# Optimization experiments

Hardware: AMD Instinct MI355X
Metric: run time of the kernel (lower is better)

Reference implementation:

```python
import jax, jax.numpy as jnp
import numpy as np

B = 2_000_000
EPS = 1e-8


def setup_inputs() -> dict:
    key = jax.random.key(0)
    k = jax.random.split(key, 6)
    loc1 = jax.random.normal(k[0], (B, 3), dtype=jnp.float32)
    loc2 = jax.random.normal(k[1], (B, 3), dtype=jnp.float32)
    # positive scales so R diag(s) R^T is PSD and the sum is invertible
    scale1 = jax.random.uniform(k[2], (B, 3), dtype=jnp.float32) + 0.1
    scale2 = jax.random.uniform(k[3], (B, 3), dtype=jnp.float32) + 0.1
    rot_matrix1 = jax.random.normal(k[4], (B, 3, 3), dtype=jnp.float32)
    rot_matrix2 = jax.random.normal(k[5], (B, 3, 3), dtype=jnp.float32)
    # cov1/cov2 are placeholders: source recomputes them when non-None
    cov1 = jnp.zeros((B, 3, 3), dtype=jnp.float32)
    cov2 = jnp.zeros((B, 3, 3), dtype=jnp.float32)
    return dict(loc1=loc1, scale1=scale1, rot_matrix1=rot_matrix1,
                loc2=loc2, scale2=scale2, rot_matrix2=rot_matrix2,
                cov1=cov1, cov2=cov2)


def _cov_from(rot, scale):
    # R @ diag(s) @ R^T, fused: einsum over the diagonal
    return jnp.einsum('bij,bj,bkj->bik', rot, scale, rot)


def reference(loc1, scale1, rot_matrix1, loc2, scale2, rot_matrix2, cov1, cov2):
    # Faithful to source: cov1/cov2 passed non-None => recomputed from rot/scale
    c1 = _cov_from(rot_matrix1, scale1)  # [B,3,3]
    c2 = _cov_from(rot_matrix2, scale2)  # [B,3,3]
    eye = jnp.eye(3, dtype=c1.dtype) * EPS
    K = jnp.matmul(c1, jnp.linalg.inv(c1 + c2 + eye))  # [B,3,3]
    # (loc2-loc1) row-vector times K^T  ==  K @ (loc2-loc1)
    loc_new = loc1 + jnp.einsum('bij,bj->bi', K, loc2 - loc1)  # [B,3]
    cov_new = c1 + jnp.matmul(K, c1)  # [B,3,3]  (sign as in source)
    return (loc_new, cov_new)
```

## Files before the change

### kernel.cpp

```cpp
#include <hip/hip_runtime.h>

#define GM_EPS 1e-8f

__global__ __launch_bounds__(256) void gaussian_merge_kernel(
    const float* __restrict__ loc1,
    const float* __restrict__ scale1,
    const float* __restrict__ rot1,
    const float* __restrict__ loc2,
    const float* __restrict__ scale2,
    const float* __restrict__ rot2,
    float* __restrict__ out_loc,
    float* __restrict__ out_cov,
    int n)
{
    int i = blockIdx.x * blockDim.x + threadIdx.x;
    if (i >= n) return;

    const long ib3 = (long)i * 3;
    const long ib9 = (long)i * 9;

    float l1[3], l2[3], s1[3], s2[3];
#pragma unroll
    for (int k = 0; k < 3; ++k) {
        l1[k] = loc1[ib3 + k];
        l2[k] = loc2[ib3 + k];
        s1[k] = scale1[ib3 + k];
        s2[k] = scale2[ib3 + k];
    }
    float R1[9], R2[9];
#pragma unroll
    for (int k = 0; k < 9; ++k) {
        R1[k] = rot1[ib9 + k];
        R2[k] = rot2[ib9 + k];
    }

    float c1[3][3], S[3][3];
#pragma unroll
    for (int a = 0; a < 3; ++a) {
#pragma unroll
        for (int b = 0; b < 3; ++b) {
            float v1 = 0.f, v2 = 0.f;
#pragma unroll
            for (int k = 0; k < 3; ++k) {
                v1 = fmaf(R1[a * 3 + k] * s1[k], R1[b * 3 + k], v1);
                v2 = fmaf(R2[a * 3 + k] * s2[k], R2[b * 3 + k], v2);
            }
            c1[a][b] = v1;
            S[a][b]  = v1 + v2 + (a == b ? GM_EPS : 0.f);
        }
    }

    const float m00 = S[0][0], m01 = S[0][1], m02 = S[0][2];
    const float m11 = S[1][1], m12 = S[1][2], m22 = S[2][2];
    const float A0 = m11 * m22 - m12 * m12;
    const float A1 = m02 * m12 - m01 * m22;
    const float A2 = m01 * m12 - m02 * m11;
    const float det = m00 * A0 + m01 * A1 + m02 * A2;
    const float invdet = 1.0f / det;

    float Sinv[3][3];
    Sinv[0][0] = A0 * invdet;
    Sinv[0][1] = A1 * invdet;
    Sinv[0][2] = A2 * invdet;
    Sinv[1][1] = (m00 * m22 - m02 * m02) * invdet;
    Sinv[1][2] = (m01 * m02 - m00 * m12) * invdet;
    Sinv[2][2] = (m00 * m11 - m01 * m01) * invdet;
    Sinv[1][0] = Sinv[0][1];
    Sinv[2][0] = Sinv[0][2];
    Sinv[2][1] = Sinv[1][2];

    float K[3][3];
#pragma unroll
    for (int a = 0; a < 3; ++a) {
#pragma unroll
        for (int b = 0; b < 3; ++b) {
            float v = 0.f;
#pragma unroll
            for (int k = 0; k < 3; ++k)
                v = fmaf(c1[a][k], Sinv[k][b], v);
            K[a][b] = v;
        }
    }

    float d0 = l2[0] - l1[0], d1 = l2[1] - l1[1], d2 = l2[2] - l1[2];
#pragma unroll
    for (int a = 0; a < 3; ++a) {
        float v = fmaf(K[a][0], d0, fmaf(K[a][1], d1, K[a][2] * d2));
        out_loc[ib3 + a] = l1[a] + v;
    }

#pragma unroll
    for (int a = 0; a < 3; ++a) {
#pragma unroll
        for (int b = 0; b < 3; ++b) {
            float v = 0.f;
#pragma unroll
            for (int k = 0; k < 3; ++k)
                v = fmaf(K[a][k], c1[k][b], v);
            out_cov[ib9 + a * 3 + b] = c1[a][b] + v;
        }
    }
}

extern "C" void kernel_launch(void* const* d_in, const int* in_sizes, int n_in,
                              void* d_out, int out_size, void* d_ws, size_t ws_size,
                              hipStream_t stream) {
    const float* loc1   = (const float*)d_in[0];
    const float* scale1 = (const float*)d_in[1];
    const float* rot1   = (const float*)d_in[2];
    const float* loc2   = (const float*)d_in[3];
    const float* scale2 = (const float*)d_in[4];
    const float* rot2   = (const float*)d_in[5];

    const int n = in_sizes[0] / 3;

    float* out     = (float*)d_out;
    float* out_loc = out;
    float* out_cov = out + (size_t)n * 3;

    const int block = 256;
    const int grid  = (n + block - 1) / block;
    gaussian_merge_kernel<<<grid, block, 0, stream>>>(
        loc1, scale1, rot1, loc2, scale2, rot2, out_loc, out_cov, n);
}
```

Before: 328.0 us.

## Stage AoS inputs and outputs through LDS with coalesced float4 transfers

Each block now loads its slice of rotations, locations and scales into shared memory with coalesced float4 loads, computes per-thread from LDS, writes results back to LDS, and stores them out with coalesced float4 stores. This replaces the strided per-thread scalar loads and stores over 3- and 9-float records, which waste memory transactions. Block size drops to 128 to bound the LDS footprint. The cost is two barriers and extra LDS traffic, plus possible bank conflicts from the stride-9 and stride-3 LDS accesses.

```diff
diff --git a/kernel.cpp b/kernel.cpp
--- a/kernel.cpp
+++ b/kernel.cpp
@@ -1,8 +1,9 @@
 #include <hip/hip_runtime.h>
 
 #define GM_EPS 1e-8f
+#define BLK 128
 
-__global__ __launch_bounds__(256) void gaussian_merge_kernel(
+__global__ __launch_bounds__(BLK) void gaussian_merge_kernel(
     const float* __restrict__ loc1,
     const float* __restrict__ scale1,
     const float* __restrict__ rot1,
@@ -13,92 +14,141 @@
     float* __restrict__ out_cov,
     int n)
 {
-    int i = blockIdx.x * blockDim.x + threadIdx.x;
-    if (i >= n) return;
+    __shared__ alignas(16) float sR1[BLK * 9];
+    __shared__ alignas(16) float sR2[BLK * 9];
+    __shared__ alignas(16) float sL1[BLK * 3];
+    __shared__ alignas(16) float sL2[BLK * 3];
+    __shared__ alignas(16) float sS1[BLK * 3];
+    __shared__ alignas(16) float sS2[BLK * 3];
 
-    const long ib3 = (long)i * 3;
-    const long ib9 = (long)i * 9;
+    const int  tid       = threadIdx.x;
+    const long blockBase = (long)blockIdx.x * BLK;
+    const int  cnt       = (int)((blockBase + BLK <= (long)n) ? BLK : ((long)n - blockBase));
 
-    float l1[3], l2[3], s1[3], s2[3];
-#pragma unroll
-    for (int k = 0; k < 3; ++k) {
-        l1[k] = loc1[ib3 + k];
-        l2[k] = loc2[ib3 + k];
-        s1[k] = scale1[ib3 + k];
-        s2[k] = scale2[ib3 + k];
-    }
-    float R1[9], R2[9];
-#pragma unroll
-    for (int k = 0; k < 9; ++k) {
-        R1[k] = rot1[ib9 + k];
-        R2[k] = rot2[ib9 + k];
-    }
+    if (cnt == BLK) {
+        const float4* r1 = (const float4*)(rot1 + blockBase * 9);
+        const float4* r2 = (const float4*)(rot2 + blockBase * 9);
+        float4* d1 = (float4*)sR1;
+        float4* d2 = (float4*)sR2;
+        for (int j = tid; j < BLK * 9 / 4; j += BLK) { d1[j] = r1[j]; d2[j] = r2[j]; }
 
-    float c1[3][3], S[3][3];
-#pragma unroll
-    for (int a = 0; a < 3; ++a) {
-#pragma unroll
-        for (int b = 0; b < 3; ++b) {
-            float v1 = 0.f, v2 = 0.f;
-#pragma unroll
-            for (int k = 0; k < 3; ++k) {
-                v1 = fmaf(R1[a * 3 + k] * s1[k], R1[b * 3 + k], v1);
-                v2 = fmaf(R2[a * 3 + k] * s2[k], R2[b * 3 + k], v2);
-            }
-            c1[a][b] = v1;
-            S[a][b]  = v1 + v2 + (a == b ? GM_EPS : 0.f);
+        const float4* p1 = (const float4*)(loc1   + blockBase * 3);
+        const float4* p2 = (const float4*)(loc2   + blockBase * 3);
+        const float4* q1 = (const float4*)(scale1 + blockBase * 3);
+        const float4* q2 = (const float4*)(scale2 + blockBase * 3);
+        float4* e1 = (float4*)sL1;
+        float4* e2 = (float4*)sL2;
+        float4* f1 = (float4*)sS1;
+        float4* f2 = (float4*)sS2;
+        if (tid < BLK * 3 / 4) {
+            e1[tid] = p1[tid]; e2[tid] = p2[tid];
+            f1[tid] = q1[tid]; f2[tid] = q2[tid];
+        }
+    } else {
+        for (int j = tid; j < cnt * 9; j += BLK) {
+            sR1[j] = rot1[blockBase * 9 + j];
+            sR2[j] = rot2[blockBase * 9 + j];
+        }
+        for (int j = tid; j < cnt * 3; j += BLK) {
+            sL1[j] = loc1[blockBase * 3 + j];
+            sL2[j] = loc2[blockBase * 3 + j];
+            sS1[j] = scale1[blockBase * 3 + j];
+            sS2[j] = scale2[blockBase * 3 + j];
         }
     }
+    __syncthreads();
 
-    const float m00 = S[0][0], m01 = S[0][1], m02 = S[0][2];
-    const float m11 = S[1][1], m12 = S[1][2], m22 = S[2][2];
-    const float A0 = m11 * m22 - m12 * m12;
-    const float A1 = m02 * m12 - m01 * m22;
-    const float A2 = m01 * m12 - m02 * m11;
-    const float det = m00 * A0 + m01 * A1 + m02 * A2;
-    const float invdet = 1.0f / det;
+    if (tid < cnt) {
+        float R1[9], R2[9], l1[3], l2[3], s1[3], s2[3];
+#pragma unroll
+        for (int k = 0; k < 9; ++k) { R1[k] = sR1[tid * 9 + k]; R2[k] = sR2[tid * 9 + k]; }
+#pragma unroll
+        for (int k = 0; k < 3; ++k) {
+            l1[k] = sL1[tid * 3 + k];
+            l2[k] = sL2[tid * 3 + k];
+            s1[k] = sS1[tid * 3 + k];
+            s2[k] = sS2[tid * 3 + k];
+        }
 
-    float Sinv[3][3];
-    Sinv[0][0] = A0 * invdet;
-    Sinv[0][1] = A1 * invdet;
-    Sinv[0][2] = A2 * invdet;
-    Sinv[1][1] = (m00 * m22 - m02 * m02) * invdet;
-    Sinv[1][2] = (m01 * m02 - m00 * m12) * invdet;
-    Sinv[2][2] = (m00 * m11 - m01 * m01) * invdet;
-    Sinv[1][0] = Sinv[0][1];
-    Sinv[2][0] = Sinv[0][2];
-    Sinv[2][1] = Sinv[1][2];
+        float c1[3][3], S[3][3];
+#pragma unroll
+        for (int a = 0; a < 3; ++a) {
+#pragma unroll
+            for (int b = 0; b < 3; ++b) {
+                float v1 = 0.f, v2 = 0.f;
+#pragma unroll
+                for (int k = 0; k < 3; ++k) {
+                    v1 = fmaf(R1[a * 3 + k] * s1[k], R1[b * 3 + k], v1);
+                    v2 = fmaf(R2[a * 3 + k] * s2[k], R2[b * 3 + k], v2);
+                }
+                c1[a][b] = v1;
+                S[a][b]  = v1 + v2 + (a == b ? GM_EPS : 0.f);
+            }
+        }
 
-    float K[3][3];
+        const float m00 = S[0][0], m01 = S[0][1], m02 = S[0][2];
+        const float m11 = S[1][1], m12 = S[1][2], m22 = S[2][2];
+        const float A0 = m11 * m22 - m12 * m12;
+        const float A1 = m02 * m12 - m01 * m22;
+        const float A2 = m01 * m12 - m02 * m11;
+        const float det    = m00 * A0 + m01 * A1 + m02 * A2;
+        const float invdet = 1.0f / det;
+
+        float Sinv[3][3];
+        Sinv[0][0] = A0 * invdet;
+        Sinv[0][1] = A1 * invdet;
+        Sinv[0][2] = A2 * invdet;
+        Sinv[1][1] = (m00 * m22 - m02 * m02) * invdet;
+        Sinv[1][2] = (m01 * m02 - m00 * m12) * invdet;
+        Sinv[2][2] = (m00 * m11 - m01 * m01) * invdet;
+        Sinv[1][0] = Sinv[0][1];
+        Sinv[2][0] = Sinv[0][2];
+        Sinv[2][1] = Sinv[1][2];
+
+        float K[3][3];
 #pragma unroll
-    for (int a = 0; a < 3; ++a) {
+        for (int a = 0; a < 3; ++a) {
 #pragma unroll
-        for (int b = 0; b < 3; ++b) {
-            float v = 0.f;
+            for (int b = 0; b < 3; ++b) {
+                float v = 0.f;
 #pragma unroll
-            for (int k = 0; k < 3; ++k)
-                v = fmaf(c1[a][k], Sinv[k][b], v);
-            K[a][b] = v;
+                for (int k = 0; k < 3; ++k)
+                    v = fmaf(c1[a][k], Sinv[k][b], v);
+                K[a][b] = v;
+            }
+        }
+
+        const float d0 = l2[0] - l1[0], d1 = l2[1] - l1[1], d2 = l2[2] - l1[2];
+#pragma unroll
+        for (int a = 0; a < 3; ++a) {
+            float v = fmaf(K[a][0], d0, fmaf(K[a][1], d1, K[a][2] * d2));
+            sL1[tid * 3 + a] = l1[a] + v;
+        }
+
+#pragma unroll
+        for (int a = 0; a < 3; ++a) {
+#pragma unroll
+            for (int b = 0; b < 3; ++b) {
+                float v = 0.f;
+#pragma unroll
+                for (int k = 0; k < 3; ++k)
+                    v = fmaf(K[a][k], c1[k][b], v);
+                sR1[tid * 9 + a * 3 + b] = c1[a][b] + v;
+            }
         }
     }
+    __syncthreads();
 
-    float d0 = l2[0] - l1[0], d1 = l2[1] - l1[1], d2 = l2[2] - l1[2];
-#pragma unroll
-    for (int a = 0; a < 3; ++a) {
-        float v = fmaf(K[a][0], d0, fmaf(K[a][1], d1, K[a][2] * d2));
-        out_loc[ib3 + a] = l1[a] + v;
-    }
-
-#pragma unroll
-    for (int a = 0; a < 3; ++a) {
-#pragma unroll
-        for (int b = 0; b < 3; ++b) {
-            float v = 0.f;
-#pragma unroll
-            for (int k = 0; k < 3; ++k)
-                v = fmaf(K[a][k], c1[k][b], v);
-            out_cov[ib9 + a * 3 + b] = c1[a][b] + v;
-        }
+    if (cnt == BLK) {
+        float4* ol = (float4*)(out_loc + blockBase * 3);
+        float4* oc = (float4*)(out_cov + blockBase * 9);
+        const float4* sl = (const float4*)sL1;
+        const float4* sc = (const float4*)sR1;
+        for (int j = tid; j < BLK * 9 / 4; j += BLK) oc[j] = sc[j];
+        if (tid < BLK * 3 / 4) ol[tid] = sl[tid];
+    } else {
+        for (int j = tid; j < cnt * 9; j += BLK) out_cov[blockBase * 9 + j] = sR1[j];
+        for (int j = tid; j < cnt * 3; j += BLK) out_loc[blockBase * 3 + j] = sL1[j];
     }
 }
 
@@ -118,8 +168,7 @@
     float* out_loc = out;
     float* out_cov = out + (size_t)n * 3;
 
-    const int block = 256;
-    const int grid  = (n + block - 1) / block;
-    gaussian_merge_kernel<<<grid, block, 0, stream>>>(
+    const int grid = (n + BLK - 1) / BLK;
+    gaussian_merge_kernel<<<grid, BLK, 0, stream>>>(
         loc1, scale1, rot1, loc2, scale2, rot2, out_loc, out_cov, n);
 }
```

Measured after the change: 331.3 us. Within noise of the previous version (+1.0%).

## Stage tiles through LDS with float4 loads, register prefetch, and persistent grid

Applied to the files above, without the earlier changes.

Rewrites the kernel as a persistent grid-stride loop over 128-element tiles. Each block loads its tile's inputs with coalesced float4 reads into shared memory, prefetching the next tile into registers while computing the current one. Outputs are staged in shared memory and written with coalesced nontemporal float4 stores. The goal is to replace the strided per-thread scalar global accesses (stride 9/3 floats) with fully coalesced vector transfers, at the cost of added LDS traffic, syncs and register pressure, plus a separate tail kernel for the remainder.

```diff
diff --git a/kernel.cpp b/kernel.cpp
--- a/kernel.cpp
+++ b/kernel.cpp
@@ -1,8 +1,31 @@
 #include <hip/hip_runtime.h>
 
 #define GM_EPS 1e-8f
-
-__global__ __launch_bounds__(256) void gaussian_merge_kernel(
+#define TILE 128
+#define NT4  960
+#define OUT4 384
+#define GRID 1792
+
+typedef float f4 __attribute__((ext_vector_type(4)));
+
+__device__ __forceinline__ f4 load_in(
+    const f4* __restrict__ r1, const f4* __restrict__ r2,
+    const f4* __restrict__ p1, const f4* __restrict__ p2,
+    const f4* __restrict__ q1, const f4* __restrict__ q2,
+    long t, int k)
+{
+    const f4* p;
+    long off;
+    if (k < 288)      { p = r1; off = t * 288 + k; }
+    else if (k < 576) { p = r2; off = t * 288 + (k - 288); }
+    else if (k < 672) { p = p1; off = t * 96  + (k - 576); }
+    else if (k < 768) { p = p2; off = t * 96  + (k - 672); }
+    else if (k < 864) { p = q1; off = t * 96  + (k - 768); }
+    else              { p = q2; off = t * 96  + (k - 864); }
+    return p[off];
+}
+
+__global__ __launch_bounds__(TILE) void gaussian_merge_kernel(
     const float* __restrict__ loc1,
     const float* __restrict__ scale1,
     const float* __restrict__ rot1,
@@ -11,95 +34,196 @@
     const float* __restrict__ rot2,
     float* __restrict__ out_loc,
     float* __restrict__ out_cov,
-    int n)
+    int nTiles)
 {
-    int i = blockIdx.x * blockDim.x + threadIdx.x;
+    __shared__ alignas(16) f4    sIn[NT4];
+    __shared__ alignas(16) float sOut[TILE * 12];
+
+    const int tid = threadIdx.x;
+
+    const f4* r1 = (const f4*)rot1;
+    const f4* r2 = (const f4*)rot2;
+    const f4* p1 = (const f4*)loc1;
+    const f4* p2 = (const f4*)loc2;
+    const f4* q1 = (const f4*)scale1;
+    const f4* q2 = (const f4*)scale2;
+
+    long t = blockIdx.x;
+    f4 pre[8];
+    if (t < nTiles) {
+#pragma unroll
+        for (int u = 0; u < 8; ++u) {
+            int k = tid + TILE * u;
+            if (k < NT4) pre[u] = load_in(r1, r2, p1, p2, q1, q2, t, k);
+        }
+    }
+
+    for (; t < nTiles; t += gridDim.x) {
+#pragma unroll
+        for (int u = 0; u < 8; ++u) {
+            int k = tid + TILE * u;
+            if (k < NT4) sIn[k] = pre[u];
+        }
+        __syncthreads();
+
+        const long tn = t + gridDim.x;
+        if (tn < nTiles) {
+#pragma unroll
+            for (int u = 0; u < 8; ++u) {
+                int k = tid + TILE * u;
+                if (k < NT4) pre[u] = load_in(r1, r2, p1, p2, q1, q2, tn, k);
+            }
+        }
+
+        {
+            const float* sInf = (const float*)sIn;
+            float R1[9], R2[9], l1[3], l2[3], s1[3], s2[3];
+#pragma unroll
+            for (int k = 0; k < 9; ++k) {
+                R1[k] = sInf[tid * 9 + k];
+                R2[k] = sInf[1152 + tid * 9 + k];
+            }
+#pragma unroll
+            for (int k = 0; k < 3; ++k) {
+                l1[k] = sInf[2304 + tid * 3 + k];
+                l2[k] = sInf[2688 + tid * 3 + k];
+                s1[k] = sInf[3072 + tid * 3 + k];
+                s2[k] = sInf[3456 + tid * 3 + k];
+            }
+
+            float c1[3][3], S[3][3];
+#pragma unroll
+            for (int a = 0; a < 3; ++a) {
+#pragma unroll
+                for (int b = 0; b < 3; ++b) {
+                    float v1 = 0.f, v2 = 0.f;
+#pragma unroll
+                    for (int k = 0; k < 3; ++k) {
+                        v1 = fmaf(R1[a * 3 + k] * s1[k], R1[b * 3 + k], v1);
+                        v2 = fmaf(R2[a * 3 + k] * s2[k], R2[b * 3 + k], v2);
+                    }
+                    c1[a][b] = v1;
+                    S[a][b]  = v1 + v2 + (a == b ? GM_EPS : 0.f);
+                }
+            }
+
+            const float m00 = S[0][0], m01 = S[0][1], m02 = S[0][2];
+            const float m11 = S[1][1], m12 = S[1][2], m22 = S[2][2];
+            const float A0 = m11 * m22 - m12 * m12;
+            const float A1 = m02 * m12 - m01 * m22;
+            const float A2 = m01 * m12 - m02 * m11;
+            const float det    = m00 * A0 + m01 * A1 + m02 * A2;
+            const float invdet = 1.0f / det;
+
+            float Sinv[3][3];
+            Sinv[0][0] = A0 * invdet;
+            Sinv[0][1] = A1 * invdet;
+            Sinv[0][2] = A2 * invdet;
+            Sinv[1][1] = (m00 * m22 - m02 * m02) * invdet;
+            Sinv[1][2] = (m01 * m02 - m00 * m12) * invdet;
+            Sinv[2][2] = (m00 * m11 - m01 * m01) * invdet;
+            Sinv[1][0] = Sinv[0][1];
+            Sinv[2][0] = Sinv[0][2];
+            Sinv[2][1] = Sinv[1][2];
+
+            float K[3][3];
+#pragma unroll
+            for (int a = 0; a < 3; ++a) {
+#pragma unroll
+                for (int b = 0; b < 3; ++b) {
+                    float v = 0.f;
+#pragma unroll
+                    for (int k = 0; k < 3; ++k)
+                        v = fmaf(c1[a][k], Sinv[k][b], v);
+                    K[a][b] = v;
+                }
+            }
+
+            const float d0 = l2[0] - l1[0], d1 = l2[1] - l1[1], d2 = l2[2] - l1[2];
+#pragma unroll
+            for (int a = 0; a < 3; ++a) {
+                float v = fmaf(K[a][0], d0, fmaf(K[a][1], d1, K[a][2] * d2));
+                sOut[tid * 3 + a] = l1[a] + v;
+            }
+
+#pragma unroll
+            for (int a = 0; a < 3; ++a) {
+#pragma unroll
+                for (int b = 0; b < 3; ++b) {
+                    float v = 0.f;
+#pragma unroll
+                    for (int k = 0; k < 3; ++k)
+                        v = fmaf(K[a][k], c1[k][b], v);
+                    sOut[384 + tid * 9 + a * 3 + b] = c1[a][b] + v;
+                }
+            }
+        }
+        __syncthreads();
+
+#pragma unroll
+        for (int w = 0; w < 3; ++w) {
+            int j = tid + TILE * w;
+            f4 v = ((const f4*)sOut)[j];
+            if (j < 96) __builtin_nontemporal_store(v, (f4*)out_loc + t * 96 + j);
+            else        __builtin_nontemporal_store(v, (f4*)out_cov + t * 288 + (j - 96));
+        }
+    }
+}
+
+__global__ void gaussian_merge_tail(
+    const float* __restrict__ loc1, const float* __restrict__ scale1,
+    const float* __restrict__ rot1, const float* __restrict__ loc2,
+    const float* __restrict__ scale2, const float* __restrict__ rot2,
+    float* __restrict__ out_loc, float* __restrict__ out_cov,
+    int start, int n)
+{
+    int i = start + blockIdx.x * blockDim.x + threadIdx.x;
     if (i >= n) return;
-
-    const long ib3 = (long)i * 3;
-    const long ib9 = (long)i * 9;
-
-    float l1[3], l2[3], s1[3], s2[3];
-#pragma unroll
+    const long ib3 = (long)i * 3, ib9 = (long)i * 9;
+    float R1[9], R2[9], l1[3], l2[3], s1[3], s2[3];
+    for (int k = 0; k < 9; ++k) { R1[k] = rot1[ib9 + k]; R2[k] = rot2[ib9 + k]; }
     for (int k = 0; k < 3; ++k) {
-        l1[k] = loc1[ib3 + k];
-        l2[k] = loc2[ib3 + k];
-        s1[k] = scale1[ib3 + k];
-        s2[k] = scale2[ib3 + k];
-    }
-    float R1[9], R2[9];
-#pragma unroll
-    for (int k = 0; k < 9; ++k) {
-        R1[k] = rot1[ib9 + k];
-        R2[k] = rot2[ib9 + k];
-    }
-
+        l1[k] = loc1[ib3 + k]; l2[k] = loc2[ib3 + k];
+        s1[k] = scale1[ib3 + k]; s2[k] = scale2[ib3 + k];
+    }
     float c1[3][3], S[3][3];
-#pragma unroll
-    for (int a = 0; a < 3; ++a) {
-#pragma unroll
+    for (int a = 0; a < 3; ++a)
         for (int b = 0; b < 3; ++b) {
             float v1 = 0.f, v2 = 0.f;
-#pragma unroll
             for (int k = 0; k < 3; ++k) {
                 v1 = fmaf(R1[a * 3 + k] * s1[k], R1[b * 3 + k], v1);
                 v2 = fmaf(R2[a * 3 + k] * s2[k], R2[b * 3 + k], v2);
             }
-            c1[a][b] = v1;
-            S[a][b]  = v1 + v2 + (a == b ? GM_EPS : 0.f);
-        }
-    }
-
+            c1[a][b] = v1; S[a][b] = v1 + v2 + (a == b ? GM_EPS : 0.f);
+        }
     const float m00 = S[0][0], m01 = S[0][1], m02 = S[0][2];
     const float m11 = S[1][1], m12 = S[1][2], m22 = S[2][2];
     const float A0 = m11 * m22 - m12 * m12;
     const float A1 = m02 * m12 - m01 * m22;
     const float A2 = m01 * m12 - m02 * m11;
-    const float det = m00 * A0 + m01 * A1 + m02 * A2;
-    const float invdet = 1.0f / det;
-
-    float Sinv[3][3];
-    Sinv[0][0] = A0 * invdet;
-    Sinv[0][1] = A1 * invdet;
-    Sinv[0][2] = A2 * invdet;
-    Sinv[1][1] = (m00 * m22 - m02 * m02) * invdet;
-    Sinv[1][2] = (m01 * m02 - m00 * m12) * invdet;
-    Sinv[2][2] = (m00 * m11 - m01 * m01) * invdet;
-    Sinv[1][0] = Sinv[0][1];
-    Sinv[2][0] = Sinv[0][2];
-    Sinv[2][1] = Sinv[1][2];
-
+    const float invdet = 1.0f / (m00 * A0 + m01 * A1 + m02 * A2);
+    float Si[3][3];
+    Si[0][0] = A0 * invdet; Si[0][1] = A1 * invdet; Si[0][2] = A2 * invdet;
+    Si[1][1] = (m00 * m22 - m02 * m02) * invdet;
+    Si[1][2] = (m01 * m02 - m00 * m12) * invdet;
+    Si[2][2] = (m00 * m11 - m01 * m01) * invdet;
+    Si[1][0] = Si[0][1]; Si[2][0] = Si[0][2]; Si[2][1] = Si[1][2];
     float K[3][3];
-#pragma unroll
-    for (int a = 0; a < 3; ++a) {
-#pragma unroll
+    for (int a = 0; a < 3; ++a)
         for (int b = 0; b < 3; ++b) {
             float v = 0.f;
-#pragma unroll
-            for (int k = 0; k < 3; ++k)
-                v = fmaf(c1[a][k], Sinv[k][b], v);
+            for (int k = 0; k < 3; ++k) v = fmaf(c1[a][k], Si[k][b], v);
             K[a][b] = v;
         }
-    }
-
-    float d0 = l2[0] - l1[0], d1 = l2[1] - l1[1], d2 = l2[2] - l1[2];
-#pragma unroll
-    for (int a = 0; a < 3; ++a) {
-        float v = fmaf(K[a][0], d0, fmaf(K[a][1], d1, K[a][2] * d2));
-        out_loc[ib3 + a] = l1[a] + v;
-    }
-
-#pragma unroll
-    for (int a = 0; a < 3; ++a) {
-#pragma unroll
+    const float d0 = l2[0] - l1[0], d1 = l2[1] - l1[1], d2 = l2[2] - l1[2];
+    for (int a = 0; a < 3; ++a)
+        out_loc[ib3 + a] = l1[a] + fmaf(K[a][0], d0, fmaf(K[a][1], d1, K[a][2] * d2));
+    for (int a = 0; a < 3; ++a)
         for (int b = 0; b < 3; ++b) {
             float v = 0.f;
-#pragma unroll
-            for (int k = 0; k < 3; ++k)
-                v = fmaf(K[a][k], c1[k][b], v);
+            for (int k = 0; k < 3; ++k) v = fmaf(K[a][k], c1[k][b], v);
             out_cov[ib9 + a * 3 + b] = c1[a][b] + v;
         }
-    }
 }
 
 extern "C" void kernel_launch(void* const* d_in, const int* in_sizes, int n_in,
@@ -118,8 +242,17 @@
     float* out_loc = out;
     float* out_cov = out + (size_t)n * 3;
 
-    const int block = 256;
-    const int grid  = (n + block - 1) / block;
-    gaussian_merge_kernel<<<grid, block, 0, stream>>>(
-        loc1, scale1, rot1, loc2, scale2, rot2, out_loc, out_cov, n);
-}
+    const int nTiles = n / TILE;
+    const int rem    = n - nTiles * TILE;
+
+    if (nTiles > 0) {
+        const int grid = (nTiles < GRID) ? nTiles : GRID;
+        gaussian_merge_kernel<<<grid, TILE, 0, stream>>>(
+            loc1, scale1, rot1, loc2, scale2, rot2, out_loc, out_cov, nTiles);
+    }
+    if (rem > 0) {
+        gaussian_merge_tail<<<(rem + 63) / 64, 64, 0, stream>>>(
+            loc1, scale1, rot1, loc2, scale2, rot2, out_loc, out_cov,
+            nTiles * TILE, n);
+    }
+}
```

After: 337.8 us. +3.0%, slower.
